# Kernel tuning notes

Measured on AMD Instinct MI355X. Metric: run time of the kernel, lower is better.

The kernel has to match this reference:

```python
import jax, jax.numpy as jnp
import numpy as np
from jax import lax

GAMMA = 1.0
BIG = 1e8  # matches the torch init value 100000000.0


def setup_inputs() -> dict:
    key = jax.random.key(0)
    k1, k2 = jax.random.split(key)
    B, n, m, d = 256, 256, 256, 32
    x = jax.random.normal(k1, (B, n, d), dtype=jnp.float32)
    y = jax.random.normal(k2, (B, m, d), dtype=jnp.float32)
    return {"x": x, "y": y}


def _soft_dtw(x, y, gamma):
    B, n, d = x.shape
    m = y.shape[1]
    # squared euclidean distances, (B, n, m); GEMM form avoids the (B,n,m,d) blowup
    x2 = jnp.sum(x * x, axis=-1)
    y2 = jnp.sum(y * y, axis=-1)
    dist = x2[:, :, None] + y2[:, None, :] - 2.0 * jnp.einsum('bnd,bmd->bnm', x, y)
    dist = jnp.maximum(dist, 0.0)  # cdist(p=2)**2 is nonnegative

    def softmin3(a, b, c):
        s = jnp.stack([a, b, c], axis=0)
        return -gamma * jax.nn.logsumexp(-s / gamma, axis=0)

    big_col = jnp.full((B,), BIG, dtype=x.dtype)

    def row_step(prev_row, d_row):
        # prev_row: (B, m+1) = D[i-1, :];  d_row: (B, m) = dist[:, i-1, :]
        def col_step(cur, inp):
            # cur: (B,) = D[i, j-1]; inp: (dist[i-1,j-1], D[i-1,j], D[i-1,j-1])
            dij, up, diag = inp
            new = dij + softmin3(up, cur, diag)
            return new, new
        xs = (d_row.T, prev_row[:, 1:].T, prev_row[:, :-1].T)  # each (m, B)
        _, vals = lax.scan(col_step, big_col, xs)  # vals: (m, B)
        new_row = jnp.concatenate([big_col[:, None], vals.T], axis=1)  # (B, m+1)
        return new_row, None

    init_row = jnp.concatenate(
        [jnp.zeros((B, 1), x.dtype), jnp.full((B, m), BIG, dtype=x.dtype)], axis=1)
    final_row, _ = lax.scan(row_step, init_row, jnp.swapaxes(dist, 0, 1))  # scan over n rows
    return jnp.mean(final_row[:, m])


def reference(x, y):
    return _soft_dtw(x, y, GAMMA)
```

## Files before the change

kernel.cpp:

```cpp
#include <hip/hip_runtime.h>

#define BIG 1e8f
#define LN2 0.69314718f
#define LOG2E 1.44269504f
#define M2L -2.8853900818f

#define RSLOT 112
#define DRB 1040

#define OFF_XH   116480
#define OFF_X2S  132864
#define OFF_Y2S  133888
#define OFF_RDY  134912
#define OFF_PRG  134976
#define LDS_BYTES 135040

typedef _Float16 half8 __attribute__((ext_vector_type(8)));
typedef _Float16 half2_t __attribute__((ext_vector_type(2)));
typedef float f32x4 __attribute__((ext_vector_type(4)));

__device__ __forceinline__ float exp2g(float x) {
#if __has_builtin(__builtin_amdgcn_exp2f)
    return __builtin_amdgcn_exp2f(x);
#else
    return exp2f(x);
#endif
}
__device__ __forceinline__ float log2g(float x) {
#if __has_builtin(__builtin_amdgcn_logf)
    return __builtin_amdgcn_logf(x);
#else
    return log2f(x);
#endif
}

__device__ __forceinline__ half2_t pkrtz(float a, float b) {
    return __builtin_bit_cast(half2_t, __builtin_amdgcn_cvt_pkrtz(a, b));
}

__device__ __forceinline__ float shfl_up1(float v, float oldv) {
    int r = __builtin_amdgcn_update_dpp(
        __builtin_bit_cast(int, oldv), __builtin_bit_cast(int, v),
        0x138 , 0xf, 0xf, false);
    return __builtin_bit_cast(float, r);
}

__device__ __forceinline__ void dec2(unsigned int w, float& a, float& b) {
    half2_t h = __builtin_bit_cast(half2_t, w);
    a = (float)h[0];
    b = (float)h[1];
}

#define MASKW0 0x7BFF7BFFu
#define MASKW1 0x70007000u
#define MASKW2 0x60006000u
#define MASKW3 0x50005000u

__global__ __launch_bounds__(128, 1) void sdtw_kernel(
    const float* __restrict__ x, const float* __restrict__ y,
    float* __restrict__ out) {
    extern __shared__ __align__(16) char smem[];
    unsigned char* band = (unsigned char*)smem;
    _Float16* xh = (_Float16*)(smem + OFF_XH);
    float* x2sL = (float*)(smem + OFF_X2S);
    float* y2sL = (float*)(smem + OFF_Y2S);
    volatile int* rdy = (volatile int*)(smem + OFF_RDY);
    volatile int* prg = (volatile int*)(smem + OFF_PRG);

    const int tid = threadIdx.x;
    const int b = blockIdx.x;
    const float* xb = x + (size_t)b * 8192;
    const float* yb = y + (size_t)b * 8192;

    {
        const uint4 mw = {MASKW0, MASKW1, MASKW2, MASKW3};
        uint4* bp = (uint4*)smem;
        for (int i = tid; i < (OFF_XH / 16); i += 128) bp[i] = mw;
    }
#pragma unroll
    for (int rr = 0; rr < 2; rr++) {
        const int r = tid + rr * 128;
        const float4* px = (const float4*)(xb + r * 32);
        union { _Float16 h[32]; half8 v[4]; } uc;
        float s2 = 0.f;
#pragma unroll
        for (int q = 0; q < 8; q++) {
            float4 f = px[q];
            s2 += f.x * f.x + f.y * f.y + f.z * f.z + f.w * f.w;
            uc.h[4 * q + 0] = (_Float16)f.x;
            uc.h[4 * q + 1] = (_Float16)f.y;
            uc.h[4 * q + 2] = (_Float16)f.z;
            uc.h[4 * q + 3] = (_Float16)f.w;
        }
        half8* dst = (half8*)&xh[r * 32];
#pragma unroll
        for (int q = 0; q < 4; q++) dst[q] = uc.v[q];
        x2sL[r] = s2 * LOG2E;

        const float4* py = (const float4*)(yb + r * 32);
        float t2 = 0.f;
#pragma unroll
        for (int q = 0; q < 8; q++) {
            float4 f = py[q];
            t2 += f.x * f.x + f.y * f.y + f.z * f.z + f.w * f.w;
        }
        y2sL[r] = t2 * LOG2E;
    }
    if (tid < 16) rdy[tid] = 0;
    if (tid == 16) *prg = 0;
    __syncthreads();

    if (tid >= 64) {
        const int lane = tid - 64;
        const int qd = lane >> 4, xr = lane & 15;

        half8 yfrag[16];
        float yvL[16];
#pragma unroll
        for (int ci = 0; ci < 16; ci++) {
            const float* yp = yb + (ci * 16 + xr) * 32 + qd * 8;
            float4 f0 = *(const float4*)yp;
            float4 f1 = *(const float4*)(yp + 4);
            half8 v;
            v[0] = (_Float16)f0.x; v[1] = (_Float16)f0.y;
            v[2] = (_Float16)f0.z; v[3] = (_Float16)f0.w;
            v[4] = (_Float16)f1.x; v[5] = (_Float16)f1.y;
            v[6] = (_Float16)f1.z; v[7] = (_Float16)f1.w;
            yfrag[ci] = v;
            yvL[ci] = y2sL[ci * 16 + xr];
        }

        for (int sg = 0; sg < 16; sg++) {
            if (sg >= 6) {
                const int need = 8 * sg - 40;
                while (*prg < need) {}
            }
            const half8 xf = *(const half8*)&xh[(sg * 16 + xr) * 32 + qd * 8];
            const float4 xl = *(const float4*)&x2sL[sg * 16 + qd * 4];
            const int p0 = 8 * sg + 2 * qd;
#pragma unroll
            for (int ci = 0; ci < 16; ci++) {
                f32x4 acc = {0.f, 0.f, 0.f, 0.f};
                acc = __builtin_amdgcn_mfma_f32_16x16x32_f16(xf, yfrag[ci], acc, 0, 0, 0);
                const int c = ci * 16 + xr;
                const float yv = yvL[ci];
                const float d0 = fmaxf(fmaf(M2L, acc[0], xl.x + yv), 0.f);
                const float d1 = fmaxf(fmaf(M2L, acc[1], xl.y + yv), 0.f);
                const float d2 = fmaxf(fmaf(M2L, acc[2], xl.z + yv), 0.f);
                const float d3 = fmaxf(fmaf(M2L, acc[3], xl.w + yv), 0.f);
                const half2_t h01 = pkrtz(d0, d1);
                const half2_t h23 = pkrtz(d2, d3);
                const int dr0 = p0 + (c >> 2);
                int s0_ = dr0;     if (s0_ >= RSLOT) s0_ -= RSLOT;
                int s1_ = dr0 + 1; if (s1_ >= RSLOT) s1_ -= RSLOT;
                *(half2_t*)&band[s0_ * DRB + 4 * c] = h01;
                *(half2_t*)&band[s1_ * DRB + 4 * c] = h23;
            }
            __threadfence_block();
            if (lane == 0) rdy[sg] = 1;
        }
        return;
    }

    const int lane = tid;
    float pBM[4], pBS[4];
    pBM[0] = BIG; pBS[0] = 1.f;
    pBM[1] = BIG; pBS[1] = 1.f;
    pBM[2] = BIG; pBS[2] = 1.f;
    pBM[3] = BIG; pBS[3] = 1.f;
    float G0M = (lane == 0) ? 0.f : BIG, G0S = 1.f;
    float MpA3 = BIG, SpA3 = 1.f, MpB3 = BIG, SpB3 = 1.f;

    float dAc[4], dBc[4];

    auto decode = [&](uint4 w) {
        dec2(w.x, dAc[0], dBc[0]);
        dec2(w.y, dAc[1], dBc[1]);
        dec2(w.z, dAc[2], dBc[2]);
        dec2(w.w, dAc[3], dBc[3]);
    };

    while (rdy[0] == 0) {}
    decode(*(const uint4*)&band[16 * lane]);

    auto step = [&](const char* gb, int koff) {
        const float MLA = shfl_up1(MpA3, BIG);
        const float MLB = shfl_up1(MpB3, BIG);
        const float SLA = shfl_up1(SpA3, 1.f);
        const float SLB = shfl_up1(SpB3, 1.f);

        const uint4 wnext = *(const uint4*)(gb + koff);

        float MA[4], xuA[4], xgA[4], xlA[4];
        {
            float ml = MLA, gm = G0M;
#pragma unroll
            for (int k = 0; k < 4; k++) {
                const float mu = fminf(fminf(pBM[k], gm), ml);
                xuA[k] = mu - pBM[k];
                xgA[k] = mu - gm;
                xlA[k] = mu - ml;
                MA[k] = dAc[k] + mu;
                ml = MA[k];
                gm = pBM[k];
            }
        }
        float euA[4], egA[4], elA[4];
#pragma unroll
        for (int k = 0; k < 4; k++) {
            euA[k] = exp2g(xuA[k]);
            egA[k] = exp2g(xgA[k]);
            elA[k] = exp2g(xlA[k]);
        }
        float MB[4], xuB[4], xgB[4], xlB[4];
        {
            float ml = MLB, gm = MLA;
#pragma unroll
            for (int k = 0; k < 4; k++) {
                const float mu = fminf(fminf(MA[k], gm), ml);
                xuB[k] = mu - MA[k];
                xgB[k] = mu - gm;
                xlB[k] = mu - ml;
                MB[k] = dBc[k] + mu;
                ml = MB[k];
                gm = MA[k];
            }
        }
        float euB[4], egB[4], elB[4];
#pragma unroll
        for (int k = 0; k < 4; k++) {
            euB[k] = exp2g(xuB[k]);
            egB[k] = exp2g(xgB[k]);
            elB[k] = exp2g(xlB[k]);
        }

        decode(wnext);

        float SA[4];
        {
            float sl = SLA, sg = G0S;
#pragma unroll
            for (int k = 0; k < 4; k++) {
                const float pre = fmaf(pBS[k], euA[k], sg * egA[k]);
                SA[k] = fmaf(sl, elA[k], pre);
                sl = SA[k];
                sg = pBS[k];
            }
        }
        float SB[4];
        {
            float sl = SLB, sg = SLA;
#pragma unroll
            for (int k = 0; k < 4; k++) {
                const float pre = fmaf(SA[k], euB[k], sg * egB[k]);
                SB[k] = fmaf(sl, elB[k], pre);
                sl = SB[k];
                sg = SA[k];
            }
        }

        MpA3 = MA[3]; SpA3 = SA[3];
        MpB3 = MB[3]; SpB3 = SB[3];
#pragma unroll
        for (int k = 0; k < 4; k++) { pBM[k] = MB[k]; pBS[k] = SB[k]; }
        G0M = MLB; G0S = SLB;
    };

    {
        const char* gb0 = (const char*)&band[16 * lane];
#pragma unroll
        for (int s_ = 1; s_ < 8; s_++) step(gb0, s_ * DRB);
    }

    for (int g = 1; g < 24; g++) {
        int st = (g > 15) ? 15 : g;
        while (rdy[st] == 0) {}
        if (lane == 0) *prg = 8 * g;
        const int s0 = 8 * g;
        const int slot0 = (s0 >= RSLOT) ? s0 - RSLOT : s0;
        const char* gb = (const char*)&band[slot0 * DRB + 16 * lane];
        if (g < 23) {
#pragma unroll
            for (int k = 0; k < 8; k++) step(gb, k * DRB);
        } else {
#pragma unroll
            for (int k = 0; k < 8; k++) step(gb, (k == 7 ? 6 : k) * DRB);
        }
    }

    if (lane == 63)
        atomicAdd(out, (MpB3 - log2g(SpB3)) * (LN2 / 256.f));
}

extern "C" void kernel_launch(void* const* d_in, const int* in_sizes, int n_in,
                              void* d_out, int out_size, void* d_ws, size_t ws_size,
                              hipStream_t stream) {
    const float* x = (const float*)d_in[0];
    const float* y = (const float*)d_in[1];
    float* out = (float*)d_out;
    const int B = in_sizes[0] / (256 * 32);

    (void)hipFuncSetAttribute((const void*)sdtw_kernel,
                              hipFuncAttributeMaxDynamicSharedMemorySize,
                              LDS_BYTES);
    (void)hipMemsetAsync(d_out, 0, sizeof(float), stream);
    sdtw_kernel<<<dim3(B), dim3(128), LDS_BYTES, stream>>>(x, y, out);
}
```

Measured before the change: 120.7 us.

## Software-pipeline the M and S recurrences across wavefront steps

Splits each anti-diagonal step so the max-track (M) recurrence for step t runs together with the scaled-sum (S) recurrence for step t-1, carrying the exp2 weights between iterations in registers. A prologue computes the first M step and an epilogue finishes the last S step before the atomic add. This shortens the serial dependency chain per step so shuffles, exp2 and FMAs from two stages can interleave. The cost is more live registers (24 extra floats) and more code.

Result: no change. 121.4 us (+0.6%).

```diff
diff --git a/kernel.cpp b/kernel.cpp
--- a/kernel.cpp
+++ b/kernel.cpp
@@ -172,6 +172,7 @@
     float MpA3 = BIG, SpA3 = 1.f, MpB3 = BIG, SpB3 = 1.f;
 
     float dAc[4], dBc[4];
+    float peuA[4], pegA[4], pelA[4], peuB[4], pegB[4], pelB[4];
 
     auto decode = [&](uint4 w) {
         dec2(w.x, dAc[0], dBc[0]);
@@ -183,14 +184,11 @@
     while (rdy[0] == 0) {}
     decode(*(const uint4*)&band[16 * lane]);
 
-    auto step = [&](const char* gb, int koff) {
+    {
+        const char* gb0 = (const char*)&band[16 * lane];
         const float MLA = shfl_up1(MpA3, BIG);
         const float MLB = shfl_up1(MpB3, BIG);
-        const float SLA = shfl_up1(SpA3, 1.f);
-        const float SLB = shfl_up1(SpB3, 1.f);
-
-        const uint4 wnext = *(const uint4*)(gb + koff);
-
+        const uint4 wnext = *(const uint4*)(gb0 + 1 * DRB);
         float MA[4], xuA[4], xgA[4], xlA[4];
         {
             float ml = MLA, gm = G0M;
@@ -205,13 +203,6 @@
                 gm = pBM[k];
             }
         }
-        float euA[4], egA[4], elA[4];
-#pragma unroll
-        for (int k = 0; k < 4; k++) {
-            euA[k] = exp2g(xuA[k]);
-            egA[k] = exp2g(xgA[k]);
-            elA[k] = exp2g(xlA[k]);
-        }
         float MB[4], xuB[4], xgB[4], xlB[4];
         {
             float ml = MLB, gm = MLA;
@@ -226,23 +217,77 @@
                 gm = MA[k];
             }
         }
-        float euB[4], egB[4], elB[4];
 #pragma unroll
         for (int k = 0; k < 4; k++) {
+            peuA[k] = exp2g(xuA[k]);
+            pegA[k] = exp2g(xgA[k]);
+            pelA[k] = exp2g(xlA[k]);
+            peuB[k] = exp2g(xuB[k]);
+            pegB[k] = exp2g(xgB[k]);
+            pelB[k] = exp2g(xlB[k]);
+        }
+        decode(wnext);
+        MpA3 = MA[3]; MpB3 = MB[3];
+#pragma unroll
+        for (int k = 0; k < 4; k++) pBM[k] = MB[k];
+        G0M = MLB;
+    }
+
+    auto fstep = [&](const char* gb, int koff) {
+        const float MLA = shfl_up1(MpA3, BIG);
+        const float MLB = shfl_up1(MpB3, BIG);
+        const uint4 wnext = *(const uint4*)(gb + koff);
+
+        float MA[4], xuA[4], xgA[4], xlA[4];
+        {
+            float ml = MLA, gm = G0M;
+#pragma unroll
+            for (int k = 0; k < 4; k++) {
+                const float mu = fminf(fminf(pBM[k], gm), ml);
+                xuA[k] = mu - pBM[k];
+                xgA[k] = mu - gm;
+                xlA[k] = mu - ml;
+                MA[k] = dAc[k] + mu;
+                ml = MA[k];
+                gm = pBM[k];
+            }
+        }
+        float MB[4], xuB[4], xgB[4], xlB[4];
+        {
+            float ml = MLB, gm = MLA;
+#pragma unroll
+            for (int k = 0; k < 4; k++) {
+                const float mu = fminf(fminf(MA[k], gm), ml);
+                xuB[k] = mu - MA[k];
+                xgB[k] = mu - gm;
+                xlB[k] = mu - ml;
+                MB[k] = dBc[k] + mu;
+                ml = MB[k];
+                gm = MA[k];
+            }
+        }
+
+        const float SLA = shfl_up1(SpA3, 1.f);
+        const float SLB = shfl_up1(SpB3, 1.f);
+
+        float euA[4], egA[4], elA[4], euB[4], egB[4], elB[4];
+#pragma unroll
+        for (int k = 0; k < 4; k++) {
+            euA[k] = exp2g(xuA[k]);
+            egA[k] = exp2g(xgA[k]);
+            elA[k] = exp2g(xlA[k]);
             euB[k] = exp2g(xuB[k]);
             egB[k] = exp2g(xgB[k]);
             elB[k] = exp2g(xlB[k]);
         }
 
-        decode(wnext);
-
         float SA[4];
         {
             float sl = SLA, sg = G0S;
 #pragma unroll
             for (int k = 0; k < 4; k++) {
-                const float pre = fmaf(pBS[k], euA[k], sg * egA[k]);
-                SA[k] = fmaf(sl, elA[k], pre);
+                const float pre = fmaf(pBS[k], peuA[k], sg * pegA[k]);
+                SA[k] = fmaf(sl, pelA[k], pre);
                 sl = SA[k];
                 sg = pBS[k];
             }
@@ -252,24 +297,30 @@
             float sl = SLB, sg = SLA;
 #pragma unroll
             for (int k = 0; k < 4; k++) {
-                const float pre = fmaf(SA[k], euB[k], sg * egB[k]);
-                SB[k] = fmaf(sl, elB[k], pre);
+                const float pre = fmaf(SA[k], peuB[k], sg * pegB[k]);
+                SB[k] = fmaf(sl, pelB[k], pre);
                 sl = SB[k];
                 sg = SA[k];
             }
         }
 
-        MpA3 = MA[3]; SpA3 = SA[3];
-        MpB3 = MB[3]; SpB3 = SB[3];
+        decode(wnext);
+
+        MpA3 = MA[3]; MpB3 = MB[3]; G0M = MLB;
+        SpA3 = SA[3]; SpB3 = SB[3]; G0S = SLB;
 #pragma unroll
         for (int k = 0; k < 4; k++) { pBM[k] = MB[k]; pBS[k] = SB[k]; }
-        G0M = MLB; G0S = SLB;
+#pragma unroll
+        for (int k = 0; k < 4; k++) {
+            peuA[k] = euA[k]; pegA[k] = egA[k]; pelA[k] = elA[k];
+            peuB[k] = euB[k]; pegB[k] = egB[k]; pelB[k] = elB[k];
+        }
     };
 
     {
         const char* gb0 = (const char*)&band[16 * lane];
 #pragma unroll
-        for (int s_ = 1; s_ < 8; s_++) step(gb0, s_ * DRB);
+        for (int s_ = 2; s_ < 8; s_++) fstep(gb0, s_ * DRB);
     }
 
     for (int g = 1; g < 24; g++) {
@@ -281,15 +332,43 @@
         const char* gb = (const char*)&band[slot0 * DRB + 16 * lane];
         if (g < 23) {
 #pragma unroll
-            for (int k = 0; k < 8; k++) step(gb, k * DRB);
+            for (int k = 0; k < 8; k++) fstep(gb, k * DRB);
         } else {
 #pragma unroll
-            for (int k = 0; k < 8; k++) step(gb, (k == 7 ? 6 : k) * DRB);
-        }
-    }
-
-    if (lane == 63)
-        atomicAdd(out, (MpB3 - log2g(SpB3)) * (LN2 / 256.f));
+            for (int k = 0; k < 8; k++) fstep(gb, (k == 7 ? 6 : k) * DRB);
+        }
+    }
+
+    {
+        const float SLA = shfl_up1(SpA3, 1.f);
+        const float SLB = shfl_up1(SpB3, 1.f);
+        float SA[4];
+        {
+            float sl = SLA, sg = G0S;
+#pragma unroll
+            for (int k = 0; k < 4; k++) {
+                const float pre = fmaf(pBS[k], peuA[k], sg * pegA[k]);
+                SA[k] = fmaf(sl, pelA[k], pre);
+                sl = SA[k];
+                sg = pBS[k];
+            }
+        }
+        float SB3;
+        {
+            float sl = SLB, sg = SLA;
+            float sbk;
+#pragma unroll
+            for (int k = 0; k < 4; k++) {
+                const float pre = fmaf(SA[k], peuB[k], sg * pegB[k]);
+                sbk = fmaf(sl, pelB[k], pre);
+                sl = sbk;
+                sg = SA[k];
+            }
+            SB3 = sbk;
+        }
+        if (lane == 63)
+            atomicAdd(out, (MpB3 - log2g(SB3)) * (LN2 / 256.f));
+    }
 }
 
 extern "C" void kernel_launch(void* const* d_in, const int* in_sizes, int n_in,
```
